# Performance work log

Measured on AMD Instinct MI355X. Metric: run time of the kernel, lower is better.

The kernel has to match this reference:

```python
import jax, jax.numpy as jnp
import numpy as np

N_NODES = 100000
N_EDGES = 1_600_000
F_IN, HID, N_CLS = 128, 64, 32
NEG_SLOPE = 0.2  # PyG GATv2Conv default


def _segment_softmax(scores, seg, num_segments):
    # numerically stable softmax over edges grouped by destination node
    m = jax.ops.segment_max(scores, seg, num_segments=num_segments)
    ex = jnp.exp(scores - m[seg])
    s = jax.ops.segment_sum(ex, seg, num_segments=num_segments)
    return ex / (s[seg] + 1e-16)


def _gatv2_layer(x, src, dst, Wl, bl, Wr, br, att, bias, num_nodes):
    xl = x @ Wl + bl              # source transform  [N, C]
    xr = x @ Wr + br              # target transform  [N, C]
    # per-edge GATv2 attention logit: a . leaky_relu(xl_j + xr_i)
    e = jax.nn.leaky_relu(xl[src] + xr[dst], NEG_SLOPE) @ att  # [E]
    alpha = _segment_softmax(e, dst, num_nodes)                 # [E]
    out = jax.ops.segment_sum(alpha[:, None] * xl[src], dst, num_segments=num_nodes)
    return out + bias


def _add_self_loops(edge_index, n):
    loops = jnp.arange(n, dtype=edge_index.dtype)
    return jnp.concatenate([edge_index, jnp.stack([loops, loops])], axis=1)


def setup_inputs() -> dict:
    key = jax.random.key(0)
    ks = jax.random.split(key, 8)
    s1 = 1.0 / np.sqrt(F_IN)
    s2 = 1.0 / np.sqrt(HID)
    return {
        "x": jax.random.normal(ks[0], (N_NODES, F_IN), jnp.float32),
        "edge_index": jax.random.randint(ks[1], (2, N_EDGES), 0, N_NODES, jnp.int64),
        "W1l": jax.random.normal(ks[2], (F_IN, HID), jnp.float32) * s1,
        "b1l": jnp.zeros((HID,), jnp.float32),
        "W1r": jax.random.normal(ks[3], (F_IN, HID), jnp.float32) * s1,
        "b1r": jnp.zeros((HID,), jnp.float32),
        "att1": jax.random.normal(ks[4], (HID,), jnp.float32) * s2,
        "bias1": jnp.zeros((HID,), jnp.float32),
        "W2l": jax.random.normal(ks[5], (HID, N_CLS), jnp.float32) * s2,
        "b2l": jnp.zeros((N_CLS,), jnp.float32),
        "W2r": jax.random.normal(ks[6], (HID, N_CLS), jnp.float32) * s2,
        "b2r": jnp.zeros((N_CLS,), jnp.float32),
        "att2": jax.random.normal(ks[7], (N_CLS,), jnp.float32) / np.sqrt(N_CLS),
        "bias2": jnp.zeros((N_CLS,), jnp.float32),
    }


def reference(x, edge_index, W1l, b1l, W1r, b1r, att1, bias1,
              W2l, b2l, W2r, b2r, att2, bias2):
    n = x.shape[0]
    ei = _add_self_loops(edge_index, n)
    src, dst = ei[0], ei[1]
    h = jax.nn.relu(_gatv2_layer(x, src, dst, W1l, b1l, W1r, b1r, att1, bias1, n))
    # F.dropout(training=False) is identity in eval mode
    out = _gatv2_layer(h, src, dst, W2l, b2l, W2r, b2r, att2, bias2, n)
    return out
```

## Files before the change

kernel.cpp:

```cpp
#include <hip/hip_runtime.h>
#include <math.h>

#define F_IN 128
#define HID 64
#define NCLS 32
#define NEG 0.2f
#define NBKT 256
#define CHUNK 8192

using bf8 = __attribute__((ext_vector_type(8))) short;
using f4v = __attribute__((ext_vector_type(4))) float;

__device__ __forceinline__ void f4fma(float4& a, float s, const float4& w) {
    a.x = fmaf(s, w.x, a.x);
    a.y = fmaf(s, w.y, a.y);
    a.z = fmaf(s, w.z, a.z);
    a.w = fmaf(s, w.w, a.w);
}
__device__ __forceinline__ unsigned short f2bf(float f) {
    unsigned u = __float_as_uint(f);
    return (unsigned short)((u + 0x7FFFu + ((u >> 16) & 1u)) >> 16);
}
__device__ __forceinline__ float bf2f(unsigned short h) {
    return __uint_as_float(((unsigned)h) << 16);
}


__global__ __launch_bounds__(256) void zeroBuckets(int* __restrict__ bucketSize, int BK) {
    int i = blockIdx.x * 256 + threadIdx.x;
    if (i < BK) bucketSize[i] = 0;
}

__global__ __launch_bounds__(256) void bucketHist(const int* __restrict__ ei,
                                                  int Eorig, int Etot,
                                                  int* __restrict__ bucketSize, int BK) {
    __shared__ int h[512];
    int t = threadIdx.x;
    for (int j = t; j < BK; j += 256) h[j] = 0;
    __syncthreads();
    int base = blockIdx.x * CHUNK;
    int end = base + CHUNK < Etot ? base + CHUNK : Etot;
    for (int i = base + t; i < end; i += 256) {
        int dst = i < Eorig ? ei[Eorig + i] : i - Eorig;
        atomicAdd(&h[dst >> 8], 1);
    }
    __syncthreads();
    for (int j = t; j < BK; j += 256)
        if (h[j]) atomicAdd(&bucketSize[j], h[j]);
}

__global__ __launch_bounds__(256) void bucketScan(const int* __restrict__ bucketSize,
                                                  int* __restrict__ bucketStart,
                                                  int* __restrict__ bucketCursor,
                                                  int BK, int Etot) {
    __shared__ int sd[256];
    int t = threadIdx.x;
    int v0 = (2 * t     < BK) ? bucketSize[2 * t]     : 0;
    int v1 = (2 * t + 1 < BK) ? bucketSize[2 * t + 1] : 0;
    int ts = v0 + v1;
    sd[t] = ts;
    __syncthreads();
    for (int off = 1; off < 256; off <<= 1) {
        int x = (t >= off) ? sd[t - off] : 0;
        __syncthreads();
        sd[t] += x;
        __syncthreads();
    }
    int excl = sd[t] - ts;
    if (2 * t < BK)     { bucketStart[2 * t] = excl;          bucketCursor[2 * t] = excl; }
    if (2 * t + 1 < BK) { bucketStart[2 * t + 1] = excl + v0; bucketCursor[2 * t + 1] = excl + v0; }
    if (t == 255) bucketStart[BK] = Etot;
}

__global__ __launch_bounds__(256) void bucketScatter(const int* __restrict__ ei,
                                                     int Eorig, int Etot,
                                                     int* __restrict__ bucketCursor,
                                                     int2* __restrict__ pairs, int BK) {
    __shared__ int h[512], lbase[512], hcur[512];
    int t = threadIdx.x;
    for (int j = t; j < BK; j += 256) { h[j] = 0; hcur[j] = 0; }
    __syncthreads();
    int base = blockIdx.x * CHUNK;
    int end = base + CHUNK < Etot ? base + CHUNK : Etot;
    for (int i = base + t; i < end; i += 256) {
        int dst = i < Eorig ? ei[Eorig + i] : i - Eorig;
        atomicAdd(&h[dst >> 8], 1);
    }
    __syncthreads();
    for (int j = t; j < BK; j += 256)
        lbase[j] = h[j] ? atomicAdd(&bucketCursor[j], h[j]) : 0;
    __syncthreads();
    for (int i = base + t; i < end; i += 256) {
        int src, dst;
        if (i < Eorig) { src = ei[i]; dst = ei[Eorig + i]; }
        else           { src = dst = i - Eorig; }
        int b = dst >> 8;
        int off = atomicAdd(&hcur[b], 1);
        pairs[lbase[b] + off] = make_int2(src, dst);
    }
}

__global__ __launch_bounds__(256) void bucketCSR(const int2* __restrict__ pairs,
                                                 const int* __restrict__ bucketStart,
                                                 int* __restrict__ rowstart,
                                                 int* __restrict__ cnt,
                                                 int* __restrict__ srclist, int N) {
    __shared__ int c[256], cur[256];
    int t = threadIdx.x;
    int b = blockIdx.x;
    int lo = b * NBKT;
    int eb = bucketStart[b], ee = bucketStart[b + 1];
    c[t] = 0;
    __syncthreads();
    for (int i = eb + t; i < ee; i += 256)
        atomicAdd(&c[pairs[i].y - lo], 1);
    __syncthreads();
    cur[t] = c[t];
    __syncthreads();
    for (int off = 1; off < 256; off <<= 1) {
        int x = (t >= off) ? cur[t - off] : 0;
        __syncthreads();
        cur[t] += x;
        __syncthreads();
    }
    int excl = cur[t] - c[t];
    int node = lo + t;
    if (node < N) { rowstart[node] = eb + excl; cnt[node] = c[t]; }
    __syncthreads();
    cur[t] = excl;
    __syncthreads();
    for (int i = eb + t; i < ee; i += 256) {
        int2 pr = pairs[i];
        int pos = atomicAdd(&cur[pr.y - lo], 1);
        srclist[eb + pos] = pr.x;
    }
}

__global__ __launch_bounds__(256) void prepW(const float* __restrict__ Wl,
                                             const float* __restrict__ Wr,
                                             uint4* __restrict__ wfrag) {
    int e = blockIdx.x * 256 + threadIdx.x;
    if (e >= 2048) return;
    int lane = e & 63;
    int kt = (e >> 6) & 3;
    int ct = (e >> 8) & 3;
    int mat = e >> 10;
    const float* W = mat ? Wr : Wl;
    int k0 = kt * 32 + (lane >> 4) * 8;
    int c = ct * 16 + (lane & 15);
    unsigned short h[8];
#pragma unroll
    for (int j = 0; j < 8; j++) h[j] = f2bf(W[(k0 + j) * HID + c]);
    wfrag[e] = *(uint4*)h;
}

__global__ __launch_bounds__(256) void transform1(const float* __restrict__ x,
                                                  const uint4* __restrict__ wfrag,
                                                  const float* __restrict__ bl,
                                                  const float* __restrict__ br,
                                                  const float* __restrict__ att,
                                                  unsigned short* __restrict__ xlb,
                                                  float* __restrict__ xr,
                                                  float* __restrict__ sl, int N) {
    __shared__ uint4 sw[2048];
    int t = threadIdx.x;
#pragma unroll
    for (int j = 0; j < 8; j++) sw[t + j * 256] = wfrag[t + j * 256];
    __syncthreads();

    int w = t >> 6, lane = t & 63;
    int nb = blockIdx.x * 64 + w * 16;
    int m = lane & 15, quad = lane >> 4;

    int arow = nb + m; if (arow >= N) arow = N - 1;
    const float* xrow = x + (size_t)arow * F_IN + quad * 8;
    bf8 afr[4];
#pragma unroll
    for (int kt = 0; kt < 4; kt++) {
        float4 lo = *(const float4*)(xrow + kt * 32);
        float4 hi = *(const float4*)(xrow + kt * 32 + 4);
        unsigned short hh[8];
        hh[0] = f2bf(lo.x); hh[1] = f2bf(lo.y); hh[2] = f2bf(lo.z); hh[3] = f2bf(lo.w);
        hh[4] = f2bf(hi.x); hh[5] = f2bf(hi.y); hh[6] = f2bf(hi.z); hh[7] = f2bf(hi.w);
        afr[kt] = *(bf8*)hh;
    }

    float am[4];
#pragma unroll
    for (int ct = 0; ct < 4; ct++) am[ct] = att[ct * 16 + m];
    float slp[4] = {0.f, 0.f, 0.f, 0.f};

#pragma unroll
    for (int mat = 0; mat < 2; mat++) {
        const float* bias = mat ? br : bl;
#pragma unroll
        for (int ct = 0; ct < 4; ct++) {
            f4v acc = {0.f, 0.f, 0.f, 0.f};
#pragma unroll
            for (int kt = 0; kt < 4; kt++) {
                bf8 bfr = *(bf8*)&sw[((mat * 4 + ct) * 4 + kt) * 64 + lane];
                acc = __builtin_amdgcn_mfma_f32_16x16x32_bf16(afr[kt], bfr, acc, 0, 0, 0);
            }
            int ch = ct * 16 + m;
            float bv = bias[ch];
#pragma unroll
            for (int reg = 0; reg < 4; reg++) {
                int node = nb + quad * 4 + reg;
                float o = acc[reg] + bv;
                if (mat) {
                    if (node < N) xr[(size_t)node * HID + ch] = o;
                } else {
                    unsigned short hb = f2bf(o);
                    slp[reg] = fmaf(am[ct], bf2f(hb), slp[reg]);
                    if (node < N) xlb[(size_t)node * HID + ch] = hb;
                }
            }
        }
    }
#pragma unroll
    for (int o2 = 1; o2 < 16; o2 <<= 1) {
#pragma unroll
        for (int reg = 0; reg < 4; reg++) slp[reg] += __shfl_xor(slp[reg], o2, 64);
    }
    if (m == 0) {
#pragma unroll
        for (int reg = 0; reg < 4; reg++) {
            int node = nb + quad * 4 + reg;
            if (node < N) sl[node] = 0.6f * slp[reg];
        }
    }
}

__global__ __launch_bounds__(256) void transform2(const float* __restrict__ h,
                                                  const float* __restrict__ Wl,
                                                  const float* __restrict__ bl,
                                                  const float* __restrict__ Wr,
                                                  const float* __restrict__ br,
                                                  const float* __restrict__ att,
                                                  unsigned short* __restrict__ xlb,
                                                  float* __restrict__ xr,
                                                  float* __restrict__ sl, int N) {
    __shared__ float sWl[HID * NCLS];
    __shared__ float sWr[HID * NCLS];
    __shared__ float sx[128][68];
    int t = threadIdx.x;
    int nb = blockIdx.x * 128;

#pragma unroll
    for (int j = 0; j < 2; j++) {
        int f = t + j * 256;
        ((float4*)sWl)[f] = ((const float4*)Wl)[f];
        ((float4*)sWr)[f] = ((const float4*)Wr)[f];
    }
    int maxf = (N - nb) * 16;
#pragma unroll
    for (int j = 0; j < 8; j++) {
        int f = t + j * 256;
        int node = f >> 4, kc = f & 15;
        float4 v = {0.f, 0.f, 0.f, 0.f};
        if (f < maxf) v = ((const float4*)(h + (size_t)nb * HID))[f];
        v.x = fmaxf(v.x, 0.f);
        v.y = fmaxf(v.y, 0.f);
        v.z = fmaxf(v.z, 0.f);
        v.w = fmaxf(v.w, 0.f);
        *(float4*)&sx[node][kc * 4] = v;
    }
    __syncthreads();

    int c4 = (t & 7) * 4;
    int slot = t >> 3;
    float4 bl4 = *(const float4*)(bl + c4);
    float4 br4 = *(const float4*)(br + c4);
    float4 at4 = *(const float4*)(att + c4);
    float4 accl[4] = {bl4, bl4, bl4, bl4};
    float4 accr[4] = {br4, br4, br4, br4};

#pragma unroll 4
    for (int k4 = 0; k4 < HID / 4; k4++) {
        int k = k4 * 4;
        float4 wl0 = *(const float4*)&sWl[(k + 0) * NCLS + c4];
        float4 wl1 = *(const float4*)&sWl[(k + 1) * NCLS + c4];
        float4 wl2 = *(const float4*)&sWl[(k + 2) * NCLS + c4];
        float4 wl3 = *(const float4*)&sWl[(k + 3) * NCLS + c4];
        float4 wr0 = *(const float4*)&sWr[(k + 0) * NCLS + c4];
        float4 wr1 = *(const float4*)&sWr[(k + 1) * NCLS + c4];
        float4 wr2 = *(const float4*)&sWr[(k + 2) * NCLS + c4];
        float4 wr3 = *(const float4*)&sWr[(k + 3) * NCLS + c4];
#pragma unroll
        for (int j = 0; j < 4; j++) {
            float4 xv = *(const float4*)&sx[slot + j * 32][k];
            f4fma(accl[j], xv.x, wl0); f4fma(accr[j], xv.x, wr0);
            f4fma(accl[j], xv.y, wl1); f4fma(accr[j], xv.y, wr1);
            f4fma(accl[j], xv.z, wl2); f4fma(accr[j], xv.z, wr2);
            f4fma(accl[j], xv.w, wl3); f4fma(accr[j], xv.w, wr3);
        }
    }
#pragma unroll
    for (int j = 0; j < 4; j++) {
        ushort4 o;
        o.x = f2bf(accl[j].x); o.y = f2bf(accl[j].y);
        o.z = f2bf(accl[j].z); o.w = f2bf(accl[j].w);
        float slpj = fmaf(at4.x, bf2f(o.x),
                     fmaf(at4.y, bf2f(o.y),
                     fmaf(at4.z, bf2f(o.z), at4.w * bf2f(o.w))));
        slpj += __shfl_xor(slpj, 1, 64);
        slpj += __shfl_xor(slpj, 2, 64);
        slpj += __shfl_xor(slpj, 4, 64);
        int g = nb + slot + j * 32;
        if (g < N) {
            *(ushort4*)(xlb + (size_t)g * NCLS + c4) = o;
            *(float4*)(xr + (size_t)g * NCLS + c4) = accr[j];
            if ((t & 7) == 0) sl[g] = 0.6f * slpj;
        }
    }
}

template <int C>
__global__ __launch_bounds__(256) void fusedAggB(const unsigned short* __restrict__ xlb,
                                                 const float* __restrict__ xr,
                                                 const float* __restrict__ sl,
                                                 const float* __restrict__ att,
                                                 const int* __restrict__ rowstart,
                                                 const int* __restrict__ cnt,
                                                 const int* __restrict__ srclist,
                                                 const float* __restrict__ bias,
                                                 float* __restrict__ out, int N) {
    const int LPQ = C / 8;
    const int SLOTS = 64 / LPQ;
    int wid = threadIdx.x >> 6;
    int lane = threadIdx.x & 63;
    int n = blockIdx.x * 4 + wid;
    if (n >= N) return;

    int slot = lane / LPQ;
    int pos = lane % LPQ;
    int c8 = pos * 8;

    float xr8[8], at8[8];
    *(float4*)&xr8[0] = *(const float4*)(xr + (size_t)n * C + c8);
    *(float4*)&xr8[4] = *(const float4*)(xr + (size_t)n * C + c8 + 4);
    *(float4*)&at8[0] = *(const float4*)(att + c8);
    *(float4*)&at8[4] = *(const float4*)(att + c8 + 4);

    float srp = 0.f;
#pragma unroll
    for (int c = 0; c < 8; c++) srp = fmaf(at8[c], xr8[c], srp);
#pragma unroll
    for (int o = 1; o < LPQ; o <<= 1) srp += __shfl_xor(srp, o, 64);
    float sr06 = 0.6f * srp;

    int row = rowstart[n];
    int deg = cnt[n];

    float s = 0.f;
    float acc[8] = {0.f, 0.f, 0.f, 0.f, 0.f, 0.f, 0.f, 0.f};

    for (int cb = 0; cb < deg; cb += 64) {
        int len = deg - cb; if (len > 64) len = 64;
        int li = lane < len ? lane : len - 1;
        int srcreg = srclist[row + cb + li];
        int nbatch = (len + SLOTS - 1) / SLOTS;
#pragma unroll 4
        for (int b = 0; b < nbatch; b++) {
            int eidx = b * SLOTS + slot;
            int src = __shfl(srcreg, eidx, 64);
            float sl06 = sl[src];
            uint4 q = *(const uint4*)(xlb + (size_t)src * C + c8);
            float v[8];
            v[0] = __uint_as_float(q.x << 16);
            v[1] = __uint_as_float(q.x & 0xffff0000u);
            v[2] = __uint_as_float(q.y << 16);
            v[3] = __uint_as_float(q.y & 0xffff0000u);
            v[4] = __uint_as_float(q.z << 16);
            v[5] = __uint_as_float(q.z & 0xffff0000u);
            v[6] = __uint_as_float(q.w << 16);
            v[7] = __uint_as_float(q.w & 0xffff0000u);
            float pa = 0.f;
#pragma unroll
            for (int c = 0; c < 8; c++) {
                float u = v[c] + xr8[c];
                pa = fmaf(fabsf(u), at8[c], pa);
            }
#pragma unroll
            for (int o = 1; o < LPQ; o <<= 1) pa += __shfl_xor(pa, o, 64);
            float p = fmaf(0.4f, pa, sl06 + sr06);
            float w = (eidx < len) ? __expf(p) : 0.f;
            s += w;
#pragma unroll
            for (int c = 0; c < 8; c++) acc[c] = fmaf(w, v[c], acc[c]);
        }
    }
#pragma unroll
    for (int o = LPQ; o < 64; o <<= 1) {
#pragma unroll
        for (int c = 0; c < 8; c++) acc[c] += __shfl_xor(acc[c], o, 64);
        s += __shfl_xor(s, o, 64);
    }
    if (lane < LPQ) {
        float bi8[8];
        *(float4*)&bi8[0] = *(const float4*)(bias + c8);
        *(float4*)&bi8[4] = *(const float4*)(bias + c8 + 4);
        float inv = 1.f / (s + 1e-16f);
        float o8[8];
#pragma unroll
        for (int c = 0; c < 8; c++) o8[c] = acc[c] * inv + bi8[c];
        *(float4*)(out + (size_t)n * C + c8)     = *(float4*)&o8[0];
        *(float4*)(out + (size_t)n * C + c8 + 4) = *(float4*)&o8[4];
    }
}

extern "C" void kernel_launch(void* const* d_in, const int* in_sizes, int n_in,
                              void* d_out, int out_size, void* d_ws, size_t ws_size,
                              hipStream_t stream) {
    const float* x     = (const float*)d_in[0];
    const int*   ei    = (const int*)d_in[1];
    const float* W1l   = (const float*)d_in[2];
    const float* b1l   = (const float*)d_in[3];
    const float* W1r   = (const float*)d_in[4];
    const float* b1r   = (const float*)d_in[5];
    const float* att1  = (const float*)d_in[6];
    const float* bias1 = (const float*)d_in[7];
    const float* W2l   = (const float*)d_in[8];
    const float* b2l   = (const float*)d_in[9];
    const float* W2r   = (const float*)d_in[10];
    const float* b2r   = (const float*)d_in[11];
    const float* att2  = (const float*)d_in[12];
    const float* bias2 = (const float*)d_in[13];
    float* out = (float*)d_out;

    int N     = in_sizes[0] / F_IN;
    int Eorig = in_sizes[1] / 2;
    int Etot  = Eorig + N;
    int BK    = (N + NBKT - 1) / NBKT;

    char* p = (char*)d_ws;
    auto alloc = [&](size_t bytes) { void* r = (void*)p; p += (bytes + 255) & ~(size_t)255; return r; };
    unsigned short* xl1b = (unsigned short*)alloc((size_t)N * HID * 2);
    float* xr1     = (float*)alloc((size_t)N * HID * 4);
    float* h       = (float*)alloc((size_t)N * HID * 4);
    unsigned short* xl2b = (unsigned short*)alloc((size_t)N * NCLS * 2);
    float* xr2     = (float*)alloc((size_t)N * NCLS * 4);
    int*   cnt     = (int*)alloc((size_t)N * 4);
    int*   rowstart= (int*)alloc((size_t)N * 4);
    int*   srclist = (int*)alloc((size_t)Etot * 4);
    uint4* wfrag   = (uint4*)alloc(2048 * 16);
    float* sl1     = (float*)alloc((size_t)N * 4);
    float* sl2     = (float*)alloc((size_t)N * 4);
    int*   bucketSize   = (int*)alloc(520 * 4);
    int*   bucketStart  = (int*)alloc(520 * 4);
    int*   bucketCursor = (int*)alloc(520 * 4);
    int2*  pairs   = (int2*)xl2b;

    int nChunks = (Etot + CHUNK - 1) / CHUNK;

    zeroBuckets<<<2, 256, 0, stream>>>(bucketSize, BK);
    bucketHist<<<nChunks, 256, 0, stream>>>(ei, Eorig, Etot, bucketSize, BK);
    bucketScan<<<1, 256, 0, stream>>>(bucketSize, bucketStart, bucketCursor, BK, Etot);
    bucketScatter<<<nChunks, 256, 0, stream>>>(ei, Eorig, Etot, bucketCursor, pairs, BK);
    bucketCSR<<<BK, 256, 0, stream>>>(pairs, bucketStart, rowstart, cnt, srclist, N);

    prepW<<<8, 256, 0, stream>>>(W1l, W1r, wfrag);
    transform1<<<(N + 63) / 64, 256, 0, stream>>>(x, wfrag, b1l, b1r, att1, xl1b, xr1, sl1, N);
    fusedAggB<HID><<<(N + 3) / 4, 256, 0, stream>>>(xl1b, xr1, sl1, att1, rowstart, cnt,
                                                    srclist, bias1, h, N);

    transform2<<<(N + 127) / 128, 256, 0, stream>>>(h, W2l, b2l, W2r, b2r, att2, xl2b, xr2, sl2, N);
    fusedAggB<NCLS><<<(N + 3) / 4, 256, 0, stream>>>(xl2b, xr2, sl2, att2, rowstart, cnt,
                                                     srclist, bias2, out, N);
}
```

Baseline: 316.6 us.

## Switch node features to fp16 and use packed half math in aggregation

Stores both the source and target transformed features as fp16 instead of bf16/fp32, which halves the xr traffic. Attention scoring in the aggregation kernel now uses packed half adds with abs masking and v_dot2 fp16 dot products. Work is remapped to 8 lanes per edge for both layer widths, with the source-score loads hoisted into a per-chunk gather. The edge-pair scratch buffer moves to h. This cuts memory traffic and ALU work per edge, but risks fp16 range and precision loss, since fp16 replaces bf16's wider exponent.

```diff
diff --git a/kernel.cpp b/kernel.cpp
--- a/kernel.cpp
+++ b/kernel.cpp
@@ -1,4 +1,5 @@
 #include <hip/hip_runtime.h>
+#include <hip/hip_fp16.h>
 #include <math.h>
 
 #define F_IN 128
@@ -10,6 +11,7 @@
 
 using bf8 = __attribute__((ext_vector_type(8))) short;
 using f4v = __attribute__((ext_vector_type(4))) float;
+typedef _Float16 hv2 __attribute__((ext_vector_type(2)));
 
 __device__ __forceinline__ void f4fma(float4& a, float s, const float4& w) {
     a.x = fmaf(s, w.x, a.x);
@@ -21,8 +23,25 @@
     unsigned u = __float_as_uint(f);
     return (unsigned short)((u + 0x7FFFu + ((u >> 16) & 1u)) >> 16);
 }
-__device__ __forceinline__ float bf2f(unsigned short h) {
-    return __uint_as_float(((unsigned)h) << 16);
+__device__ __forceinline__ unsigned short f2h(float f) {
+    return __half_as_ushort(__float2half(f));
+}
+__device__ __forceinline__ float h2f(unsigned short u) {
+    return __half2float(__ushort_as_half(u));
+}
+__device__ __forceinline__ unsigned pkaddabs(unsigned a, unsigned b) {
+    hv2 r = __builtin_bit_cast(hv2, a) + __builtin_bit_cast(hv2, b);
+    return __builtin_bit_cast(unsigned, r) & 0x7FFF7FFFu;
+}
+__device__ __forceinline__ float fdot2(unsigned a, unsigned b, float c) {
+    return __builtin_amdgcn_fdot2(__builtin_bit_cast(hv2, a),
+                                  __builtin_bit_cast(hv2, b), c, false);
+}
+__device__ __forceinline__ float h2lo(unsigned a) {
+    return (float)__builtin_bit_cast(hv2, a).x;
+}
+__device__ __forceinline__ float h2hi(unsigned a) {
+    return (float)__builtin_bit_cast(hv2, a).y;
 }
 
 
@@ -138,9 +157,18 @@
 
 __global__ __launch_bounds__(256) void prepW(const float* __restrict__ Wl,
                                              const float* __restrict__ Wr,
-                                             uint4* __restrict__ wfrag) {
+                                             const float* __restrict__ att1,
+                                             const float* __restrict__ att2,
+                                             uint4* __restrict__ wfrag,
+                                             unsigned short* __restrict__ att1h,
+                                             unsigned short* __restrict__ att2h) {
     int e = blockIdx.x * 256 + threadIdx.x;
-    if (e >= 2048) return;
+    if (e >= 2048) {
+        int i = e - 2048;
+        if (i < HID) att1h[i] = f2h(att1[i]);
+        else if (i < HID + NCLS) att2h[i - HID] = f2h(att2[i - HID]);
+        return;
+    }
     int lane = e & 63;
     int kt = (e >> 6) & 3;
     int ct = (e >> 8) & 3;
@@ -159,8 +187,8 @@
                                                   const float* __restrict__ bl,
                                                   const float* __restrict__ br,
                                                   const float* __restrict__ att,
-                                                  unsigned short* __restrict__ xlb,
-                                                  float* __restrict__ xr,
+                                                  unsigned short* __restrict__ xlh,
+                                                  unsigned short* __restrict__ xrh,
                                                   float* __restrict__ sl, int N) {
     __shared__ uint4 sw[2048];
     int t = threadIdx.x;
@@ -208,11 +236,11 @@
                 int node = nb + quad * 4 + reg;
                 float o = acc[reg] + bv;
                 if (mat) {
-                    if (node < N) xr[(size_t)node * HID + ch] = o;
+                    if (node < N) xrh[(size_t)node * HID + ch] = f2h(o);
                 } else {
-                    unsigned short hb = f2bf(o);
-                    slp[reg] = fmaf(am[ct], bf2f(hb), slp[reg]);
-                    if (node < N) xlb[(size_t)node * HID + ch] = hb;
+                    unsigned short hb = f2h(o);
+                    slp[reg] = fmaf(am[ct], h2f(hb), slp[reg]);
+                    if (node < N) xlh[(size_t)node * HID + ch] = hb;
                 }
             }
         }
@@ -237,8 +265,8 @@
                                                   const float* __restrict__ Wr,
                                                   const float* __restrict__ br,
                                                   const float* __restrict__ att,
-                                                  unsigned short* __restrict__ xlb,
-                                                  float* __restrict__ xr,
+                                                  unsigned short* __restrict__ xlh,
+                                                  unsigned short* __restrict__ xrh,
                                                   float* __restrict__ sl, int N) {
     __shared__ float sWl[HID * NCLS];
     __shared__ float sWr[HID * NCLS];
@@ -298,114 +326,135 @@
 #pragma unroll
     for (int j = 0; j < 4; j++) {
         ushort4 o;
-        o.x = f2bf(accl[j].x); o.y = f2bf(accl[j].y);
-        o.z = f2bf(accl[j].z); o.w = f2bf(accl[j].w);
-        float slpj = fmaf(at4.x, bf2f(o.x),
-                     fmaf(at4.y, bf2f(o.y),
-                     fmaf(at4.z, bf2f(o.z), at4.w * bf2f(o.w))));
+        o.x = f2h(accl[j].x); o.y = f2h(accl[j].y);
+        o.z = f2h(accl[j].z); o.w = f2h(accl[j].w);
+        ushort4 orr;
+        orr.x = f2h(accr[j].x); orr.y = f2h(accr[j].y);
+        orr.z = f2h(accr[j].z); orr.w = f2h(accr[j].w);
+        float slpj = fmaf(at4.x, h2f(o.x),
+                     fmaf(at4.y, h2f(o.y),
+                     fmaf(at4.z, h2f(o.z), at4.w * h2f(o.w))));
         slpj += __shfl_xor(slpj, 1, 64);
         slpj += __shfl_xor(slpj, 2, 64);
         slpj += __shfl_xor(slpj, 4, 64);
         int g = nb + slot + j * 32;
         if (g < N) {
-            *(ushort4*)(xlb + (size_t)g * NCLS + c4) = o;
-            *(float4*)(xr + (size_t)g * NCLS + c4) = accr[j];
+            *(ushort4*)(xlh + (size_t)g * NCLS + c4) = o;
+            *(ushort4*)(xrh + (size_t)g * NCLS + c4) = orr;
             if ((t & 7) == 0) sl[g] = 0.6f * slpj;
         }
     }
 }
 
+#define AGG_BATCH(EIDX, WEXPR)                                        \
+    {                                                                 \
+        int src = __shfl(srcv, (EIDX), 64);                           \
+        float sl06 = __shfl(slv, (EIDX), 64);                         \
+        unsigned vp[NH];                                              \
+        const unsigned short* rowp = xlh + (unsigned)src * C + cb0;   \
+        if (NH == 4) *(uint4*)vp = *(const uint4*)rowp;               \
+        else         *(uint2*)vp = *(const uint2*)rowp;               \
+        float pa = 0.f;                                               \
+        _Pragma("unroll")                                             \
+        for (int j = 0; j < NH; j++)                                  \
+            pa = fdot2(pkaddabs(vp[j], xrp[j]), atp[j], pa);          \
+        pa += __shfl_xor(pa, 1, 64);                                  \
+        pa += __shfl_xor(pa, 2, 64);                                  \
+        pa += __shfl_xor(pa, 4, 64);                                  \
+        float wgt = (WEXPR);                                          \
+        s += wgt;                                                     \
+        _Pragma("unroll")                                             \
+        for (int j = 0; j < NH; j++) {                                \
+            acc[2 * j]     = fmaf(wgt, h2lo(vp[j]), acc[2 * j]);      \
+            acc[2 * j + 1] = fmaf(wgt, h2hi(vp[j]), acc[2 * j + 1]);  \
+        }                                                             \
+    }
+
 template <int C>
-__global__ __launch_bounds__(256) void fusedAggB(const unsigned short* __restrict__ xlb,
-                                                 const float* __restrict__ xr,
+__global__ __launch_bounds__(256) void fusedAggC(const unsigned short* __restrict__ xlh,
+                                                 const unsigned short* __restrict__ xrh,
+                                                 const unsigned short* __restrict__ atth,
                                                  const float* __restrict__ sl,
-                                                 const float* __restrict__ att,
                                                  const int* __restrict__ rowstart,
                                                  const int* __restrict__ cnt,
                                                  const int* __restrict__ srclist,
                                                  const float* __restrict__ bias,
                                                  float* __restrict__ out, int N) {
-    const int LPQ = C / 8;
-    const int SLOTS = 64 / LPQ;
+    constexpr int CH = C / 8;
+    constexpr int NH = CH / 2;
     int wid = threadIdx.x >> 6;
     int lane = threadIdx.x & 63;
     int n = blockIdx.x * 4 + wid;
     if (n >= N) return;
 
-    int slot = lane / LPQ;
-    int pos = lane % LPQ;
-    int c8 = pos * 8;
-
-    float xr8[8], at8[8];
-    *(float4*)&xr8[0] = *(const float4*)(xr + (size_t)n * C + c8);
-    *(float4*)&xr8[4] = *(const float4*)(xr + (size_t)n * C + c8 + 4);
-    *(float4*)&at8[0] = *(const float4*)(att + c8);
-    *(float4*)&at8[4] = *(const float4*)(att + c8 + 4);
+    int slot = lane >> 3;
+    int pos  = lane & 7;
+    int cb0  = pos * CH;
+
+    unsigned xrp[NH], atp[NH];
+    if (NH == 4) {
+        *(uint4*)xrp = *(const uint4*)(xrh + (size_t)n * C + cb0);
+        *(uint4*)atp = *(const uint4*)(atth + cb0);
+    } else {
+        *(uint2*)xrp = *(const uint2*)(xrh + (size_t)n * C + cb0);
+        *(uint2*)atp = *(const uint2*)(atth + cb0);
+    }
 
     float srp = 0.f;
 #pragma unroll
-    for (int c = 0; c < 8; c++) srp = fmaf(at8[c], xr8[c], srp);
-#pragma unroll
-    for (int o = 1; o < LPQ; o <<= 1) srp += __shfl_xor(srp, o, 64);
+    for (int j = 0; j < NH; j++) srp = fdot2(xrp[j], atp[j], srp);
+    srp += __shfl_xor(srp, 1, 64);
+    srp += __shfl_xor(srp, 2, 64);
+    srp += __shfl_xor(srp, 4, 64);
     float sr06 = 0.6f * srp;
 
     int row = rowstart[n];
     int deg = cnt[n];
 
     float s = 0.f;
-    float acc[8] = {0.f, 0.f, 0.f, 0.f, 0.f, 0.f, 0.f, 0.f};
+    float acc[CH];
+#pragma unroll
+    for (int c = 0; c < CH; c++) acc[c] = 0.f;
 
     for (int cb = 0; cb < deg; cb += 64) {
         int len = deg - cb; if (len > 64) len = 64;
         int li = lane < len ? lane : len - 1;
-        int srcreg = srclist[row + cb + li];
-        int nbatch = (len + SLOTS - 1) / SLOTS;
-#pragma unroll 4
-        for (int b = 0; b < nbatch; b++) {
-            int eidx = b * SLOTS + slot;
-            int src = __shfl(srcreg, eidx, 64);
-            float sl06 = sl[src];
-            uint4 q = *(const uint4*)(xlb + (size_t)src * C + c8);
-            float v[8];
-            v[0] = __uint_as_float(q.x << 16);
-            v[1] = __uint_as_float(q.x & 0xffff0000u);
-            v[2] = __uint_as_float(q.y << 16);
-            v[3] = __uint_as_float(q.y & 0xffff0000u);
-            v[4] = __uint_as_float(q.z << 16);
-            v[5] = __uint_as_float(q.z & 0xffff0000u);
-            v[6] = __uint_as_float(q.w << 16);
-            v[7] = __uint_as_float(q.w & 0xffff0000u);
-            float pa = 0.f;
-#pragma unroll
-            for (int c = 0; c < 8; c++) {
-                float u = v[c] + xr8[c];
-                pa = fmaf(fabsf(u), at8[c], pa);
-            }
-#pragma unroll
-            for (int o = 1; o < LPQ; o <<= 1) pa += __shfl_xor(pa, o, 64);
-            float p = fmaf(0.4f, pa, sl06 + sr06);
-            float w = (eidx < len) ? __expf(p) : 0.f;
-            s += w;
-#pragma unroll
-            for (int c = 0; c < 8; c++) acc[c] = fmaf(w, v[c], acc[c]);
-        }
-    }
-#pragma unroll
-    for (int o = LPQ; o < 64; o <<= 1) {
-#pragma unroll
-        for (int c = 0; c < 8; c++) acc[c] += __shfl_xor(acc[c], o, 64);
+        int srcv = srclist[row + cb + li];
+        float slv = sl[srcv];
+        int nfull = len >> 3, rem = len & 7;
+#pragma unroll 2
+        for (int b = 0; b < nfull; b++) {
+            AGG_BATCH(b * 8 + slot, __expf(fmaf(0.4f, pa, sl06 + sr06)))
+        }
+        if (rem) {
+            AGG_BATCH(nfull * 8 + slot,
+                      (slot < rem) ? __expf(fmaf(0.4f, pa, sl06 + sr06)) : 0.f)
+        }
+    }
+#pragma unroll
+    for (int o = 8; o < 64; o <<= 1) {
+#pragma unroll
+        for (int c = 0; c < CH; c++) acc[c] += __shfl_xor(acc[c], o, 64);
         s += __shfl_xor(s, o, 64);
     }
-    if (lane < LPQ) {
-        float bi8[8];
-        *(float4*)&bi8[0] = *(const float4*)(bias + c8);
-        *(float4*)&bi8[4] = *(const float4*)(bias + c8 + 4);
+    if (lane < 8) {
         float inv = 1.f / (s + 1e-16f);
-        float o8[8];
-#pragma unroll
-        for (int c = 0; c < 8; c++) o8[c] = acc[c] * inv + bi8[c];
-        *(float4*)(out + (size_t)n * C + c8)     = *(float4*)&o8[0];
-        *(float4*)(out + (size_t)n * C + c8 + 4) = *(float4*)&o8[4];
+        float o8[CH];
+        float bi[CH];
+        if (NH == 4) {
+            *(float4*)&bi[0] = *(const float4*)(bias + cb0);
+            *(float4*)&bi[4] = *(const float4*)(bias + cb0 + 4);
+        } else {
+            *(float4*)&bi[0] = *(const float4*)(bias + cb0);
+        }
+#pragma unroll
+        for (int c = 0; c < CH; c++) o8[c] = fmaf(acc[c], inv, bi[c]);
+        if (NH == 4) {
+            *(float4*)(out + (size_t)n * C + cb0)     = *(float4*)&o8[0];
+            *(float4*)(out + (size_t)n * C + cb0 + 4) = *(float4*)&o8[4];
+        } else {
+            *(float4*)(out + (size_t)n * C + cb0) = *(float4*)&o8[0];
+        }
     }
 }
 
@@ -435,21 +484,23 @@
 
     char* p = (char*)d_ws;
     auto alloc = [&](size_t bytes) { void* r = (void*)p; p += (bytes + 255) & ~(size_t)255; return r; };
-    unsigned short* xl1b = (unsigned short*)alloc((size_t)N * HID * 2);
-    float* xr1     = (float*)alloc((size_t)N * HID * 4);
+    unsigned short* xl1h = (unsigned short*)alloc((size_t)N * HID * 2);
+    unsigned short* xr1h = (unsigned short*)alloc((size_t)N * HID * 2);
     float* h       = (float*)alloc((size_t)N * HID * 4);
-    unsigned short* xl2b = (unsigned short*)alloc((size_t)N * NCLS * 2);
-    float* xr2     = (float*)alloc((size_t)N * NCLS * 4);
+    unsigned short* xl2h = (unsigned short*)alloc((size_t)N * NCLS * 2);
+    unsigned short* xr2h = (unsigned short*)alloc((size_t)N * NCLS * 2);
     int*   cnt     = (int*)alloc((size_t)N * 4);
     int*   rowstart= (int*)alloc((size_t)N * 4);
     int*   srclist = (int*)alloc((size_t)Etot * 4);
     uint4* wfrag   = (uint4*)alloc(2048 * 16);
     float* sl1     = (float*)alloc((size_t)N * 4);
     float* sl2     = (float*)alloc((size_t)N * 4);
+    unsigned short* att1h = (unsigned short*)alloc(HID * 2);
+    unsigned short* att2h = (unsigned short*)alloc(NCLS * 2);
     int*   bucketSize   = (int*)alloc(520 * 4);
     int*   bucketStart  = (int*)alloc(520 * 4);
     int*   bucketCursor = (int*)alloc(520 * 4);
-    int2*  pairs   = (int2*)xl2b;
+    int2*  pairs   = (int2*)h;
 
     int nChunks = (Etot + CHUNK - 1) / CHUNK;
 
@@ -459,12 +510,12 @@
     bucketScatter<<<nChunks, 256, 0, stream>>>(ei, Eorig, Etot, bucketCursor, pairs, BK);
     bucketCSR<<<BK, 256, 0, stream>>>(pairs, bucketStart, rowstart, cnt, srclist, N);
 
-    prepW<<<8, 256, 0, stream>>>(W1l, W1r, wfrag);
-    transform1<<<(N + 63) / 64, 256, 0, stream>>>(x, wfrag, b1l, b1r, att1, xl1b, xr1, sl1, N);
-    fusedAggB<HID><<<(N + 3) / 4, 256, 0, stream>>>(xl1b, xr1, sl1, att1, rowstart, cnt,
+    prepW<<<9, 256, 0, stream>>>(W1l, W1r, att1, att2, wfrag, att1h, att2h);
+    transform1<<<(N + 63) / 64, 256, 0, stream>>>(x, wfrag, b1l, b1r, att1, xl1h, xr1h, sl1, N);
+    fusedAggC<HID><<<(N + 3) / 4, 256, 0, stream>>>(xl1h, xr1h, att1h, sl1, rowstart, cnt,
                                                     srclist, bias1, h, N);
 
-    transform2<<<(N + 127) / 128, 256, 0, stream>>>(h, W2l, b2l, W2r, b2r, att2, xl2b, xr2, sl2, N);
-    fusedAggB<NCLS><<<(N + 3) / 4, 256, 0, stream>>>(xl2b, xr2, sl2, att2, rowstart, cnt,
+    transform2<<<(N + 127) / 128, 256, 0, stream>>>(h, W2l, b2l, W2r, b2r, att2, xl2h, xr2h, sl2, N);
+    fusedAggC<NCLS><<<(N + 3) / 4, 256, 0, stream>>>(xl2h, xr2h, att2h, sl2, rowstart, cnt,
                                                      srclist, bias2, out, N);
 }
```

New measurement: 317.2 us. Within noise of the previous version (+0.2%).
